# Kernel tuning notes

Hardware: AMD Instinct MI355X
Metric: run time of the kernel (lower is better)

Reference implementation:

```python
import jax, jax.numpy as jnp
import numpy as np

D_MODEL, KAN_HIDDEN, NUM, K = 1024, 128, 3, 3  # grid_size=3, spline order k=3
GRID_RANGE = (-1.0, 1.0)


def make_grid(in_dim):
    # extended grid: num+1 interior knots padded by k steps of h on each side -> num+1+2k points
    h = (GRID_RANGE[1] - GRID_RANGE[0]) / NUM
    g = jnp.arange(-K, NUM + K + 1, dtype=jnp.float32) * h + GRID_RANGE[0]  # [num+1+2k]
    return jnp.broadcast_to(g, (in_dim, g.shape[0]))  # [in_dim, G]


def b_splines(x, grid):
    # Cox-de-Boor recursion. x: [N, D], grid: [D, G] -> basis [N, D, G-1-K]
    xg = x[:, :, None]  # [N, D, 1]
    B = ((xg >= grid[None, :, :-1]) & (xg < grid[None, :, 1:])).astype(x.dtype)
    for d in range(1, K + 1):
        left = (xg - grid[None, :, : -(d + 1)]) / (grid[:, d:-1] - grid[:, : -(d + 1)])[None]
        right = (grid[None, :, d + 1:] - xg) / (grid[:, d + 1:] - grid[:, 1:-d])[None]
        B = left * B[:, :, :-1] + right * B[:, :, 1:]
    return B  # [N, D, NUM+K]


def kan_layer(x, grid, coef, scale_base, scale_sp):
    # y[n,i,o] = scale_base[i,o]*silu(x[n,i]) + scale_sp[i,o]*sum_g B[n,i,g]*coef[i,o,g]; out = y.sum(i)
    B = b_splines(x, grid)  # [N, in, NUM+K]
    spline = jnp.einsum('nig,iog->no', B, coef * scale_sp[:, :, None])
    base = jnp.einsum('ni,io->no', jax.nn.silu(x), scale_base)
    return base + spline  # [N, out]


def setup_inputs() -> dict:
    key = jax.random.key(0)
    ks = jax.random.split(key, 7)
    s = 0.1  # small init scale for spline coefficients, matching noisy init spirit
    return {
        'x': jax.random.normal(ks[0], (4, 4096, D_MODEL), dtype=jnp.float32),
        'coef1': jax.random.normal(ks[1], (D_MODEL, KAN_HIDDEN, NUM + K), dtype=jnp.float32) * s,
        'scale_base1': jax.random.normal(ks[2], (D_MODEL, KAN_HIDDEN), dtype=jnp.float32),
        'scale_sp1': jnp.ones((D_MODEL, KAN_HIDDEN), dtype=jnp.float32),
        'coef2': jax.random.normal(ks[3], (KAN_HIDDEN, D_MODEL, NUM + K), dtype=jnp.float32) * s,
        'scale_base2': jax.random.normal(ks[4], (KAN_HIDDEN, D_MODEL), dtype=jnp.float32),
        'scale_sp2': jnp.ones((KAN_HIDDEN, D_MODEL), dtype=jnp.float32),
    }


def reference(x, coef1, scale_base1, scale_sp1, coef2, scale_base2, scale_sp2):
    b, s, d = x.shape
    xf = x.reshape(-1, d)  # [N, d_model]
    g1 = make_grid(D_MODEL)
    g2 = make_grid(KAN_HIDDEN)
    y1 = kan_layer(xf, g1, coef1, scale_base1, scale_sp1)   # [N, kan_hidden]
    y2 = kan_layer(y1, g2, coef2, scale_base2, scale_sp2)   # [N, d_model]
    return y2.reshape(b, s, d)
```

## Files before the change

### kernel.cpp

```cpp
#include <hip/hip_runtime.h>
#include <stdint.h>

typedef float f32x4 __attribute__((ext_vector_type(4)));
typedef __bf16 bf16x8 __attribute__((ext_vector_type(8)));

#define NROW 16384
#define DM   1024
#define HID  128
#define K1   8192
#define K2   1024

__device__ __forceinline__ unsigned short f2bf(float f) {
  unsigned u = __builtin_bit_cast(unsigned, f);
  u += 0x7fffu + ((u >> 16) & 1u);
  return (unsigned short)(u >> 16);
}

__device__ __forceinline__ void g2l16(const void* g, void* l) {
  __builtin_amdgcn_global_load_lds(
      (const __attribute__((address_space(1))) unsigned int*)g,
      (__attribute__((address_space(3))) unsigned int*)l, 16, 0, 0);
}

__device__ __forceinline__ bf16x8 expand8(float v) {
  const float t = (v + 3.0f) * 1.5f;
  const float cf = floorf(t);
  const float u = t - cf;
  const int c = (int)cf;
  const float u2 = u * u;
  const float u3 = u2 * u;
  const float omu = 1.0f - u;
  const float p0 = u3 * (1.0f / 6.0f);
  const float p1 = (1.0f / 6.0f) + 0.5f * u + 0.5f * u2 - 0.5f * u3;
  const float p2 = (4.0f / 6.0f) - u2 + 0.5f * u3;
  const float p3 = omu * omu * omu * (1.0f / 6.0f);
  float B[6];
#pragma unroll
  for (int g = 0; g < 6; ++g) {
    const int r = c - g;
    float b = (r == 3) ? p3 : 0.0f;
    b = (r == 2) ? p2 : b;
    b = (r == 1) ? p1 : b;
    b = (r == 0) ? p0 : b;
    B[g] = b;
  }
  const float s = v * __frcp_rn(1.0f + __expf(-v));
  const __bf16 sh = (__bf16)s;
  const float slo = s - (float)sh;
  bf16x8 r8;
  r8[0] = sh;
#pragma unroll
  for (int g = 0; g < 6; ++g) r8[g + 1] = (__bf16)B[g];
  r8[7] = (__bf16)slo;
  return r8;
}

__global__ void kan_prep_w1(const float* __restrict__ c1, const float* __restrict__ sb1,
                            const float* __restrict__ sp1, unsigned short* __restrict__ w1t) {
  const int t = blockIdx.x * 256 + threadIdx.x;
  const int o = t >> 10, i = t & 1023;
  const float sb = sb1[i * HID + o], sp = sp1[i * HID + o];
  const float* cf = c1 + (size_t)(i * HID + o) * 6;
  union { uint4 u; unsigned short h[8]; } r;
  const unsigned short b = f2bf(sb);
  r.h[0] = b; r.h[7] = b;
#pragma unroll
  for (int g = 0; g < 6; ++g) r.h[g + 1] = f2bf(cf[g] * sp);
  *(uint4*)(w1t + (size_t)o * K1 + i * 8) = r.u;
}

__global__ void kan_prep_w2(const float* __restrict__ c2, const float* __restrict__ sb2,
                            const float* __restrict__ sp2, unsigned short* __restrict__ w2t) {
  const int t = blockIdx.x * 256 + threadIdx.x;
  const int o = t >> 7, i = t & 127;
  const float sb = sb2[i * DM + o], sp = sp2[i * DM + o];
  const float* cf = c2 + (size_t)(i * DM + o) * 6;
  union { uint4 u; unsigned short h[8]; } r;
  const unsigned short b = f2bf(sb);
  r.h[0] = b; r.h[7] = b;
#pragma unroll
  for (int g = 0; g < 6; ++g) r.h[g + 1] = f2bf(cf[g] * sp);
  *(uint4*)(w2t + (size_t)o * K2 + i * 8) = r.u;
}

__global__ __launch_bounds__(512, 2) void kan_gemm1(
    const float* __restrict__ x, const unsigned short* __restrict__ w1t,
    unsigned short* __restrict__ a2) {
  __shared__ __align__(16) unsigned short lds[2 * 12288];
  const int tid = threadIdx.x;
  const int lane = tid & 63, w = tid >> 6;
  const int wm = w >> 2, wn = w & 3;
  const int m0 = blockIdx.x * 64;
  const int arow = tid >> 3, acol = tid & 7;

  f32x4 acc[2][2];
#pragma unroll
  for (int a = 0; a < 2; ++a)
#pragma unroll
    for (int b = 0; b < 2; ++b) acc[a][b] = (f32x4){0.f, 0.f, 0.f, 0.f};

  const int NT = K1 / 64;

  auto stageB = [&](int kt, int buf) {
#pragma unroll
    for (int q = 0; q < 2; ++q) {
      const int g = w * 2 + q;
      const int r = g * 8 + (lane >> 3);
      const int slot = (lane & 7) ^ (lane >> 3);
      g2l16(w1t + (size_t)r * K1 + kt * 64 + slot * 8,
            (char*)lds + buf * 24576 + 8192 + g * 1024);
    }
  };
  auto stageA = [&](float xv, int buf) {
    bf16x8 u = expand8(xv);
    char* base = (char*)lds + buf * 24576;
    *(bf16x8*)(base + ((arow * 128 + acol * 16) ^ ((arow & 7) << 4))) = u;
  };

  float xv = x[(size_t)(m0 + arow) * DM + acol];
  stageB(0, 0);
  stageA(xv, 0);
  xv = x[(size_t)(m0 + arow) * DM + 8 + acol];
  __syncthreads();

  for (int kt = 0; kt < NT; ++kt) {
    const int cur = kt & 1;
    if (kt + 1 < NT) {
      stageB(kt + 1, cur ^ 1);
      stageA(xv, cur ^ 1);
      const int nk = (kt + 2 < NT) ? kt + 2 : NT - 1;
      xv = x[(size_t)(m0 + arow) * DM + nk * 8 + acol];
    }
    const char* ab = (const char*)lds + cur * 24576;
    const char* bb = ab + 8192;
#pragma unroll
    for (int ks = 0; ks < 2; ++ks) {
      bf16x8 af[2], bfr[2];
#pragma unroll
      for (int mi = 0; mi < 2; ++mi) {
        const int row = wm * 32 + mi * 16 + (lane & 15);
        af[mi] = *(const bf16x8*)(ab + ((row * 128 + ks * 64 + (lane >> 4) * 16) ^ ((row & 7) << 4)));
      }
#pragma unroll
      for (int ni = 0; ni < 2; ++ni) {
        const int col = wn * 32 + ni * 16 + (lane & 15);
        bfr[ni] = *(const bf16x8*)(bb + ((col * 128 + ks * 64 + (lane >> 4) * 16) ^ ((col & 7) << 4)));
      }
#pragma unroll
      for (int mi = 0; mi < 2; ++mi)
#pragma unroll
        for (int ni = 0; ni < 2; ++ni)
          acc[mi][ni] = __builtin_amdgcn_mfma_f32_16x16x32_bf16(af[mi], bfr[ni], acc[mi][ni], 0, 0, 0);
    }
    __syncthreads();
  }

#pragma unroll
  for (int mi = 0; mi < 2; ++mi)
#pragma unroll
    for (int r = 0; r < 4; ++r) {
      const int row = wm * 32 + mi * 16 + (lane >> 4) * 4 + r;
#pragma unroll
      for (int ni = 0; ni < 2; ++ni) {
        const int col = wn * 32 + ni * 16 + (lane & 15);
        bf16x8 u = expand8(acc[mi][ni][r]);
        *(bf16x8*)(a2 + (size_t)(m0 + row) * K2 + col * 8) = u;
      }
    }
}

__global__ __launch_bounds__(256, 2) void kan_gemm2(
    const unsigned short* __restrict__ a2, const unsigned short* __restrict__ w2t,
    float* __restrict__ out) {
  __shared__ __align__(16) unsigned short lds[2 * 16384];
  const int tid = threadIdx.x;
  const int lane = tid & 63, w = tid >> 6;
  const int wm = w >> 1, wn = w & 1;
  const int mt = blockIdx.x & 127, nt = blockIdx.x >> 7;
  const int m0 = mt * 128, n0 = nt * 128;

  f32x4 acc[4][4];
#pragma unroll
  for (int a = 0; a < 4; ++a)
#pragma unroll
    for (int b = 0; b < 4; ++b) acc[a][b] = (f32x4){0.f, 0.f, 0.f, 0.f};

  auto stage = [&](int kt, int buf) {
#pragma unroll
    for (int q = 0; q < 4; ++q) {
      const int r = (w * 4 + q) * 8 + (lane >> 3);
      const int slot = (lane & 7) ^ (lane >> 3);
      g2l16(a2 + (size_t)(m0 + r) * K2 + kt * 64 + slot * 8,
            (char*)lds + buf * 32768 + (w * 4 + q) * 1024);
      g2l16(w2t + (size_t)(n0 + r) * K2 + kt * 64 + slot * 8,
            (char*)lds + buf * 32768 + 16384 + (w * 4 + q) * 1024);
    }
  };

  stage(0, 0);
  __syncthreads();
  for (int kt = 0; kt < 16; ++kt) {
    const int cur = kt & 1;
    if (kt + 1 < 16) stage(kt + 1, cur ^ 1);
    const char* ab = (const char*)lds + cur * 32768;
    const char* bb = ab + 16384;
#pragma unroll
    for (int ks = 0; ks < 2; ++ks) {
      bf16x8 af[4], bfr[4];
#pragma unroll
      for (int mi = 0; mi < 4; ++mi) {
        const int row = wm * 64 + mi * 16 + (lane & 15);
        af[mi] = *(const bf16x8*)(ab + ((row * 128 + ks * 64 + (lane >> 4) * 16) ^ ((row & 7) << 4)));
      }
#pragma unroll
      for (int ni = 0; ni < 4; ++ni) {
        const int col = wn * 64 + ni * 16 + (lane & 15);
        bfr[ni] = *(const bf16x8*)(bb + ((col * 128 + ks * 64 + (lane >> 4) * 16) ^ ((col & 7) << 4)));
      }
#pragma unroll
      for (int mi = 0; mi < 4; ++mi)
#pragma unroll
        for (int ni = 0; ni < 4; ++ni)
          acc[mi][ni] = __builtin_amdgcn_mfma_f32_16x16x32_bf16(af[mi], bfr[ni], acc[mi][ni], 0, 0, 0);
    }
    __syncthreads();
  }

#pragma unroll
  for (int mi = 0; mi < 4; ++mi)
#pragma unroll
    for (int r = 0; r < 4; ++r) {
      const int row = wm * 64 + mi * 16 + (lane >> 4) * 4 + r;
#pragma unroll
      for (int ni = 0; ni < 4; ++ni) {
        const int col = wn * 64 + ni * 16 + (lane & 15);
        out[(size_t)(m0 + row) * DM + n0 + col] = acc[mi][ni][r];
      }
    }
}

extern "C" void kernel_launch(void* const* d_in, const int* in_sizes, int n_in,
                              void* d_out, int out_size, void* d_ws, size_t ws_size,
                              hipStream_t stream) {
  const float* x   = (const float*)d_in[0];
  const float* c1  = (const float*)d_in[1];
  const float* sb1 = (const float*)d_in[2];
  const float* sp1 = (const float*)d_in[3];
  const float* c2  = (const float*)d_in[4];
  const float* sb2 = (const float*)d_in[5];
  const float* sp2 = (const float*)d_in[6];
  float* out = (float*)d_out;

  unsigned short* w1t = (unsigned short*)d_ws;
  unsigned short* w2t = w1t + (size_t)HID * K1;
  unsigned short* a2  = w2t + (size_t)DM * K2;

  kan_prep_w1<<<512, 256, 0, stream>>>(c1, sb1, sp1, w1t);
  kan_prep_w2<<<512, 256, 0, stream>>>(c2, sb2, sp2, w2t);
  kan_gemm1<<<NROW / 64, 512, 0, stream>>>(x, w1t, a2);
  kan_gemm2<<<(NROW / 128) * (DM / 128), 256, 0, stream>>>(a2, w2t, out);
}
```

Before: 147.3 us.

## Halve gemm1 row tile and warp-specialize A expansion and B loading

The first GEMM now uses 32-row tiles, giving twice as many blocks, with a higher occupancy hint and a smaller LDS footprint. Half the waves expand x into B-spline features while the other half stream weight tiles into LDS, which separates VALU work from asynchronous loads. The aim is to raise occupancy and latency hiding on a grid that previously gave roughly one block per CU. The cost is lower MFMA reuse per wave and double the weight-tile reads from L2.

```diff
diff --git a/kernel.cpp b/kernel.cpp
--- a/kernel.cpp
+++ b/kernel.cpp
@@ -83,63 +83,67 @@
   *(uint4*)(w2t + (size_t)o * K2 + i * 8) = r.u;
 }
 
-__global__ __launch_bounds__(512, 2) void kan_gemm1(
+__global__ __launch_bounds__(512, 4) void kan_gemm1(
     const float* __restrict__ x, const unsigned short* __restrict__ w1t,
     unsigned short* __restrict__ a2) {
-  __shared__ __align__(16) unsigned short lds[2 * 12288];
+  __shared__ __align__(16) unsigned short lds[2 * 10240];
   const int tid = threadIdx.x;
   const int lane = tid & 63, w = tid >> 6;
-  const int wm = w >> 2, wn = w & 3;
-  const int m0 = blockIdx.x * 64;
+  const int wm = w & 1, wn = (w >> 1) & 3;
+  const int m0 = blockIdx.x * 32;
   const int arow = tid >> 3, acol = tid & 7;
 
-  f32x4 acc[2][2];
-#pragma unroll
-  for (int a = 0; a < 2; ++a)
-#pragma unroll
-    for (int b = 0; b < 2; ++b) acc[a][b] = (f32x4){0.f, 0.f, 0.f, 0.f};
+  f32x4 acc[2];
+  acc[0] = (f32x4){0.f, 0.f, 0.f, 0.f};
+  acc[1] = (f32x4){0.f, 0.f, 0.f, 0.f};
 
   const int NT = K1 / 64;
 
   auto stageB = [&](int kt, int buf) {
 #pragma unroll
-    for (int q = 0; q < 2; ++q) {
-      const int g = w * 2 + q;
+    for (int q = 0; q < 4; ++q) {
+      const int g = (w - 4) * 4 + q;
       const int r = g * 8 + (lane >> 3);
       const int slot = (lane & 7) ^ (lane >> 3);
       g2l16(w1t + (size_t)r * K1 + kt * 64 + slot * 8,
-            (char*)lds + buf * 24576 + 8192 + g * 1024);
+            (char*)lds + buf * 20480 + 4096 + g * 1024);
     }
   };
   auto stageA = [&](float xv, int buf) {
     bf16x8 u = expand8(xv);
-    char* base = (char*)lds + buf * 24576;
+    char* base = (char*)lds + buf * 20480;
     *(bf16x8*)(base + ((arow * 128 + acol * 16) ^ ((arow & 7) << 4))) = u;
   };
 
-  float xv = x[(size_t)(m0 + arow) * DM + acol];
-  stageB(0, 0);
-  stageA(xv, 0);
-  xv = x[(size_t)(m0 + arow) * DM + 8 + acol];
+  float xv = 0.f;
+  if (w < 4) {
+    xv = x[(size_t)(m0 + arow) * DM + acol];
+    stageA(xv, 0);
+    xv = x[(size_t)(m0 + arow) * DM + 8 + acol];
+  } else {
+    stageB(0, 0);
+  }
   __syncthreads();
 
   for (int kt = 0; kt < NT; ++kt) {
     const int cur = kt & 1;
     if (kt + 1 < NT) {
-      stageB(kt + 1, cur ^ 1);
-      stageA(xv, cur ^ 1);
-      const int nk = (kt + 2 < NT) ? kt + 2 : NT - 1;
-      xv = x[(size_t)(m0 + arow) * DM + nk * 8 + acol];
-    }
-    const char* ab = (const char*)lds + cur * 24576;
-    const char* bb = ab + 8192;
+      if (w < 4) {
+        stageA(xv, cur ^ 1);
+        const int nk = (kt + 2 < NT) ? kt + 2 : NT - 1;
+        xv = x[(size_t)(m0 + arow) * DM + nk * 8 + acol];
+      } else {
+        stageB(kt + 1, cur ^ 1);
+      }
+    }
+    const char* ab = (const char*)lds + cur * 20480;
+    const char* bb = ab + 4096;
 #pragma unroll
     for (int ks = 0; ks < 2; ++ks) {
-      bf16x8 af[2], bfr[2];
-#pragma unroll
-      for (int mi = 0; mi < 2; ++mi) {
-        const int row = wm * 32 + mi * 16 + (lane & 15);
-        af[mi] = *(const bf16x8*)(ab + ((row * 128 + ks * 64 + (lane >> 4) * 16) ^ ((row & 7) << 4)));
+      bf16x8 af, bfr[2];
+      {
+        const int row = wm * 16 + (lane & 15);
+        af = *(const bf16x8*)(ab + ((row * 128 + ks * 64 + (lane >> 4) * 16) ^ ((row & 7) << 4)));
       }
 #pragma unroll
       for (int ni = 0; ni < 2; ++ni) {
@@ -147,26 +151,22 @@
         bfr[ni] = *(const bf16x8*)(bb + ((col * 128 + ks * 64 + (lane >> 4) * 16) ^ ((col & 7) << 4)));
       }
 #pragma unroll
-      for (int mi = 0; mi < 2; ++mi)
-#pragma unroll
-        for (int ni = 0; ni < 2; ++ni)
-          acc[mi][ni] = __builtin_amdgcn_mfma_f32_16x16x32_bf16(af[mi], bfr[ni], acc[mi][ni], 0, 0, 0);
+      for (int ni = 0; ni < 2; ++ni)
+        acc[ni] = __builtin_amdgcn_mfma_f32_16x16x32_bf16(af, bfr[ni], acc[ni], 0, 0, 0);
     }
     __syncthreads();
   }
 
 #pragma unroll
-  for (int mi = 0; mi < 2; ++mi)
-#pragma unroll
-    for (int r = 0; r < 4; ++r) {
-      const int row = wm * 32 + mi * 16 + (lane >> 4) * 4 + r;
-#pragma unroll
-      for (int ni = 0; ni < 2; ++ni) {
-        const int col = wn * 32 + ni * 16 + (lane & 15);
-        bf16x8 u = expand8(acc[mi][ni][r]);
-        *(bf16x8*)(a2 + (size_t)(m0 + row) * K2 + col * 8) = u;
-      }
-    }
+  for (int r = 0; r < 4; ++r) {
+    const int row = wm * 16 + (lane >> 4) * 4 + r;
+#pragma unroll
+    for (int ni = 0; ni < 2; ++ni) {
+      const int col = wn * 32 + ni * 16 + (lane & 15);
+      bf16x8 u = expand8(acc[ni][r]);
+      *(bf16x8*)(a2 + (size_t)(m0 + row) * K2 + col * 8) = u;
+    }
+  }
 }
 
 __global__ __launch_bounds__(256, 2) void kan_gemm2(
@@ -257,6 +257,6 @@
 
   kan_prep_w1<<<512, 256, 0, stream>>>(c1, sb1, sp1, w1t);
   kan_prep_w2<<<512, 256, 0, stream>>>(c2, sb2, sp2, w2t);
-  kan_gemm1<<<NROW / 64, 512, 0, stream>>>(x, w1t, a2);
+  kan_gemm1<<<NROW / 32, 512, 0, stream>>>(x, w1t, a2);
   kan_gemm2<<<(NROW / 128) * (DM / 128), 256, 0, stream>>>(a2, w2t, out);
 }
```

New measurement: 136.7 us. -7.2%, faster.

## Restructure first KAN GEMM with split-K, register-held weights and packed spline expansion

Applied to the files above, without the earlier changes.

The first GEMM now uses 128-row tiles with the K dimension split across two blocks and across two wave groups inside each block. The weight fragments are loaded straight from global memory into registers and double-buffered there, and the in-block partial sums are reduced through LDS. A new combine kernel adds the two block partials and applies the spline expansion for the second layer. The spline basis construction is also rewritten to place the four nonzero bf16 values with 64-bit shifts instead of per-element selects. The aim is better MFMA reuse and less LDS traffic for the weights, at the cost of an extra kernel launch and an fp32 partial-sum round trip through global memory.

```diff
diff --git a/kernel.cpp b/kernel.cpp
--- a/kernel.cpp
+++ b/kernel.cpp
@@ -16,6 +16,10 @@
   return (unsigned short)(u >> 16);
 }
 
+__device__ __forceinline__ uint32_t pkbf(float lo, float hi) {
+  return (uint32_t)f2bf(lo) | ((uint32_t)f2bf(hi) << 16);
+}
+
 __device__ __forceinline__ void g2l16(const void* g, void* l) {
   __builtin_amdgcn_global_load_lds(
       (const __attribute__((address_space(1))) unsigned int*)g,
@@ -26,33 +30,33 @@
   const float t = (v + 3.0f) * 1.5f;
   const float cf = floorf(t);
   const float u = t - cf;
-  const int c = (int)cf;
-  const float u2 = u * u;
-  const float u3 = u2 * u;
-  const float omu = 1.0f - u;
+  int c = (int)cf;
+  c = c < -1 ? -1 : c;
+  c = c > 9 ? 9 : c;
+  const float u2 = u * u, u3 = u2 * u, omu = 1.0f - u;
   const float p0 = u3 * (1.0f / 6.0f);
   const float p1 = (1.0f / 6.0f) + 0.5f * u + 0.5f * u2 - 0.5f * u3;
   const float p2 = (4.0f / 6.0f) - u2 + 0.5f * u3;
   const float p3 = omu * omu * omu * (1.0f / 6.0f);
-  float B[6];
-#pragma unroll
-  for (int g = 0; g < 6; ++g) {
-    const int r = c - g;
-    float b = (r == 3) ? p3 : 0.0f;
-    b = (r == 2) ? p2 : b;
-    b = (r == 1) ? p1 : b;
-    b = (r == 0) ? p0 : b;
-    B[g] = b;
-  }
+  const uint64_t W = (uint64_t)pkbf(p3, p2) | ((uint64_t)pkbf(p1, p0) << 32);
+  const int sa = (c - 2) * 16;
+  const int sl = sa & 63;
+  const uint64_t t1 = W << sl;
+  const uint64_t t2 = (W >> (63 - sl)) >> 1;
+  const uint64_t t3 = W >> ((-sa) & 63);
+  const uint64_t L = sa < 0 ? t3 : (sa < 64 ? t1 : 0);
+  const uint64_t H = sa < 0 ? 0  : (sa < 64 ? t2 : t1);
   const float s = v * __frcp_rn(1.0f + __expf(-v));
-  const __bf16 sh = (__bf16)s;
-  const float slo = s - (float)sh;
-  bf16x8 r8;
-  r8[0] = sh;
-#pragma unroll
-  for (int g = 0; g < 6; ++g) r8[g + 1] = (__bf16)B[g];
-  r8[7] = (__bf16)slo;
-  return r8;
+  const unsigned short sh = f2bf(s);
+  const float shf = __builtin_bit_cast(float, (uint32_t)sh << 16);
+  const unsigned short slo = f2bf(s - shf);
+  const uint32_t w0 = ((uint32_t)L & 0xffff0000u) | sh;
+  const uint32_t w1 = (uint32_t)(L >> 32);
+  const uint32_t w2 = (uint32_t)H;
+  const uint32_t w3 = ((uint32_t)(H >> 32) & 0xffffu) | ((uint32_t)slo << 16);
+  union { uint4 q; bf16x8 b; } r;
+  r.q = (uint4){w0, w1, w2, w3};
+  return r.b;
 }
 
 __global__ void kan_prep_w1(const float* __restrict__ c1, const float* __restrict__ sb1,
@@ -85,88 +89,104 @@
 
 __global__ __launch_bounds__(512, 2) void kan_gemm1(
     const float* __restrict__ x, const unsigned short* __restrict__ w1t,
-    unsigned short* __restrict__ a2) {
-  __shared__ __align__(16) unsigned short lds[2 * 12288];
+    float* __restrict__ yp) {
+  __shared__ __align__(16) char lds[65536];
   const int tid = threadIdx.x;
   const int lane = tid & 63, w = tid >> 6;
-  const int wm = w >> 2, wn = w & 3;
-  const int m0 = blockIdx.x * 64;
-  const int arow = tid >> 3, acol = tid & 7;
-
-  f32x4 acc[2][2];
-#pragma unroll
-  for (int a = 0; a < 2; ++a)
-#pragma unroll
-    for (int b = 0; b < 2; ++b) acc[a][b] = (f32x4){0.f, 0.f, 0.f, 0.f};
-
-  const int NT = K1 / 64;
-
-  auto stageB = [&](int kt, int buf) {
-#pragma unroll
-    for (int q = 0; q < 2; ++q) {
-      const int g = w * 2 + q;
-      const int r = g * 8 + (lane >> 3);
-      const int slot = (lane & 7) ^ (lane >> 3);
-      g2l16(w1t + (size_t)r * K1 + kt * 64 + slot * 8,
-            (char*)lds + buf * 24576 + 8192 + g * 1024);
-    }
+  const int wk = w >> 2, wm = (w >> 1) & 1, wn = w & 1;
+  const int mt = blockIdx.x >> 1, kh = blockIdx.x & 1;
+  const int m0 = mt * 128;
+  const int arow = tid >> 2, acs = (tid & 3) * 2;
+
+  f32x4 acc[4][4];
+#pragma unroll
+  for (int a = 0; a < 4; ++a)
+#pragma unroll
+    for (int b = 0; b < 4; ++b) acc[a][b] = (f32x4){0.f, 0.f, 0.f, 0.f};
+
+  const int bo = wn * 64 + (lane & 15);
+  const int bk = wk * 32 + (lane >> 4) * 8;
+
+  auto loadB = [&](int kt, bf16x8* bfrag) {
+#pragma unroll
+    for (int ni = 0; ni < 4; ++ni)
+      bfrag[ni] = *(const bf16x8*)(w1t + (size_t)(bo + ni * 16) * K1 + kh * 4096 + kt * 64 + bk);
   };
-  auto stageA = [&](float xv, int buf) {
-    bf16x8 u = expand8(xv);
-    char* base = (char*)lds + buf * 24576;
-    *(bf16x8*)(base + ((arow * 128 + acol * 16) ^ ((arow & 7) << 4))) = u;
+  auto stageA = [&](float2 xv, int buf) {
+    bf16x8 u0 = expand8(xv.x);
+    bf16x8 u1 = expand8(xv.y);
+    char* base = lds + buf * 16384;
+    const int sw = (arow & 7) << 4;
+    *(bf16x8*)(base + ((arow * 128 + acs * 16) ^ sw)) = u0;
+    *(bf16x8*)(base + ((arow * 128 + acs * 16 + 16) ^ sw)) = u1;
   };
 
-  float xv = x[(size_t)(m0 + arow) * DM + acol];
-  stageB(0, 0);
+  const float* xrow = x + (size_t)(m0 + arow) * DM + kh * 512 + acs;
+  bf16x8 bcur[4], bnxt[4];
+  float2 xv = *(const float2*)xrow;
+  loadB(0, bcur);
   stageA(xv, 0);
-  xv = x[(size_t)(m0 + arow) * DM + 8 + acol];
+  xv = *(const float2*)(xrow + 8);
   __syncthreads();
 
+  const int NT = 64;
   for (int kt = 0; kt < NT; ++kt) {
     const int cur = kt & 1;
     if (kt + 1 < NT) {
-      stageB(kt + 1, cur ^ 1);
+      loadB(kt + 1, bnxt);
       stageA(xv, cur ^ 1);
-      const int nk = (kt + 2 < NT) ? kt + 2 : NT - 1;
-      xv = x[(size_t)(m0 + arow) * DM + nk * 8 + acol];
-    }
-    const char* ab = (const char*)lds + cur * 24576;
-    const char* bb = ab + 8192;
-#pragma unroll
-    for (int ks = 0; ks < 2; ++ks) {
-      bf16x8 af[2], bfr[2];
-#pragma unroll
-      for (int mi = 0; mi < 2; ++mi) {
-        const int row = wm * 32 + mi * 16 + (lane & 15);
-        af[mi] = *(const bf16x8*)(ab + ((row * 128 + ks * 64 + (lane >> 4) * 16) ^ ((row & 7) << 4)));
-      }
-#pragma unroll
-      for (int ni = 0; ni < 2; ++ni) {
-        const int col = wn * 32 + ni * 16 + (lane & 15);
-        bfr[ni] = *(const bf16x8*)(bb + ((col * 128 + ks * 64 + (lane >> 4) * 16) ^ ((col & 7) << 4)));
-      }
-#pragma unroll
-      for (int mi = 0; mi < 2; ++mi)
-#pragma unroll
-        for (int ni = 0; ni < 2; ++ni)
-          acc[mi][ni] = __builtin_amdgcn_mfma_f32_16x16x32_bf16(af[mi], bfr[ni], acc[mi][ni], 0, 0, 0);
-    }
+      if (kt + 2 < NT) xv = *(const float2*)(xrow + (kt + 2) * 8);
+    }
+    const char* ab = lds + cur * 16384;
+    bf16x8 af[4];
+#pragma unroll
+    for (int mi = 0; mi < 4; ++mi) {
+      const int row = wm * 64 + mi * 16 + (lane & 15);
+      af[mi] = *(const bf16x8*)(ab + ((row * 128 + wk * 64 + (lane >> 4) * 16) ^ ((row & 7) << 4)));
+    }
+#pragma unroll
+    for (int mi = 0; mi < 4; ++mi)
+#pragma unroll
+      for (int ni = 0; ni < 4; ++ni)
+        acc[mi][ni] = __builtin_amdgcn_mfma_f32_16x16x32_bf16(af[mi], bcur[ni], acc[mi][ni], 0, 0, 0);
     __syncthreads();
-  }
-
-#pragma unroll
-  for (int mi = 0; mi < 2; ++mi)
-#pragma unroll
-    for (int r = 0; r < 4; ++r) {
-      const int row = wm * 32 + mi * 16 + (lane >> 4) * 4 + r;
-#pragma unroll
-      for (int ni = 0; ni < 2; ++ni) {
-        const int col = wn * 32 + ni * 16 + (lane & 15);
-        bf16x8 u = expand8(acc[mi][ni][r]);
-        *(bf16x8*)(a2 + (size_t)(m0 + row) * K2 + col * 8) = u;
-      }
-    }
+#pragma unroll
+    for (int ni = 0; ni < 4; ++ni) bcur[ni] = bnxt[ni];
+  }
+
+  if (wk == 1) {
+    char* r = lds + (w & 3) * 16384;
+#pragma unroll
+    for (int mi = 0; mi < 4; ++mi)
+#pragma unroll
+      for (int ni = 0; ni < 4; ++ni)
+        *(f32x4*)(r + (mi * 4 + ni) * 1024 + lane * 16) = acc[mi][ni];
+  }
+  __syncthreads();
+  if (wk == 0) {
+    const char* r = lds + w * 16384;
+    float* yb = yp + (size_t)kh * NROW * HID;
+#pragma unroll
+    for (int mi = 0; mi < 4; ++mi)
+#pragma unroll
+      for (int ni = 0; ni < 4; ++ni) {
+        f32x4 o = *(const f32x4*)(r + (mi * 4 + ni) * 1024 + lane * 16);
+        o += acc[mi][ni];
+        const int col = wn * 64 + ni * 16 + (lane & 15);
+#pragma unroll
+        for (int rr = 0; rr < 4; ++rr) {
+          const int row = wm * 64 + mi * 16 + (lane >> 4) * 4 + rr;
+          yb[(size_t)(m0 + row) * HID + col] = o[rr];
+        }
+      }
+  }
+}
+
+__global__ void kan_combine(const float* __restrict__ yp, unsigned short* __restrict__ a2) {
+  const size_t i = (size_t)blockIdx.x * 256 + threadIdx.x;
+  const float v = yp[i] + yp[i + (size_t)NROW * HID];
+  bf16x8 u = expand8(v);
+  *(bf16x8*)(a2 + i * 8) = u;
 }
 
 __global__ __launch_bounds__(256, 2) void kan_gemm2(
@@ -254,9 +274,11 @@
   unsigned short* w1t = (unsigned short*)d_ws;
   unsigned short* w2t = w1t + (size_t)HID * K1;
   unsigned short* a2  = w2t + (size_t)DM * K2;
+  float*          yp  = (float*)(a2 + (size_t)NROW * K2);
 
   kan_prep_w1<<<512, 256, 0, stream>>>(c1, sb1, sp1, w1t);
   kan_prep_w2<<<512, 256, 0, stream>>>(c2, sb2, sp2, w2t);
-  kan_gemm1<<<NROW / 64, 512, 0, stream>>>(x, w1t, a2);
+  kan_gemm1<<<256, 512, 0, stream>>>(x, w1t, yp);
+  kan_combine<<<NROW * HID / 256, 256, 0, stream>>>(yp, a2);
   kan_gemm2<<<(NROW / 128) * (DM / 128), 256, 0, stream>>>(a2, w2t, out);
 }
```

Measured after the change: 130.5 us. 1.13x faster.
